# Kernel optimization log

Measured on AMD Instinct MI355X. Metric: run time of the kernel, lower is better.

Reference implementation:

```python
import jax, jax.numpy as jnp
import numpy as np
from jax import lax

K = 3
STRIDE = 1
PAD = 1


def _active_sites(mask):
    # mask: [B, Cm, H, W] int. A patch is 'active' if ANY element of the
    # unfolded (im2col) patch is nonzero -> max-pool of (mask != 0) over the
    # same kernel/stride/padding window.
    m = jnp.any(mask != 0, axis=1, keepdims=True).astype(jnp.float32)  # [B,1,H,W]
    pooled = lax.reduce_window(
        m, 0.0, lax.max,
        window_dimensions=(1, 1, K, K),
        window_strides=(1, 1, STRIDE, STRIDE),
        padding=((0, 0), (0, 0), (PAD, PAD), (PAD, PAD)))
    return pooled > 0  # [B,1,H_out,W_out] bool


def reference(x, mask, weight, bias):
    # Faithful math of MyConv: conv2d(x, weight) + bias at active patch sites
    # (patches whose mask window contains any nonzero), exact zeros elsewhere.
    # masked_scatter in the original preserves patch order, so this equals
    # active * (conv + bias).
    conv = lax.conv_general_dilated(
        x, weight,
        window_strides=(STRIDE, STRIDE),
        padding=((PAD, PAD), (PAD, PAD)),
        dimension_numbers=('NCHW', 'OIHW', 'NCHW'))  # [B,C_out,H_out,W_out]
    active = _active_sites(mask)
    out = (conv + bias[None, :, None, None]) * active.astype(conv.dtype)
    return out


def setup_inputs() -> dict:
    key = jax.random.key(0)
    k1, k2, k3, k4 = jax.random.split(key, 4)
    B, C_in, C_out, H, W = 8, 128, 128, 128, 128
    x = jax.random.normal(k1, (B, C_in, H, W), dtype=jnp.float32)
    mask = jax.random.randint(k2, (B, 1, H, W), 0, 2, dtype=jnp.int32)
    fan_in = C_in * K * K
    bound = 1.0 / np.sqrt(fan_in)
    weight = jax.random.uniform(k3, (C_out, C_in, K, K), minval=-bound, maxval=bound, dtype=jnp.float32)
    bias = jax.random.uniform(k4, (C_out,), minval=-bound, maxval=bound, dtype=jnp.float32)
    return {"x": x, "mask": mask, "weight": weight, "bias": bias}
```

## Files before the change

### kernel.cpp

```cpp
#include <hip/hip_runtime.h>


typedef __bf16 bf16x8 __attribute__((ext_vector_type(8)));
typedef unsigned short u16x8 __attribute__((ext_vector_type(8)));
typedef float f32x4 __attribute__((ext_vector_type(4)));

__device__ __forceinline__ unsigned short f2bf(float f) {
    unsigned int u = __float_as_uint(f);
    u += 0x7fffu + ((u >> 16) & 1u);
    return (unsigned short)(u >> 16);
}

__global__ void cvt_x2(const float* __restrict__ x, unsigned short* __restrict__ xp) {
    const int t   = threadIdx.x;
    const int b   = blockIdx.x / 130;
    const int hh2 = blockIdx.x % 130;
    unsigned short* dst = xp + (size_t)((b * 130 + hh2) * 4) * 4160;
    const u16x8 z = {0, 0, 0, 0, 0, 0, 0, 0};
    if (hh2 == 0 || hh2 == 129) {
        for (int i = t; i < 2080; i += 256) ((u16x8*)dst)[i] = z;
        return;
    }
    const int h  = hh2 - 1;
    const int hf = t >> 7;
    const int w  = t & 127;
    #pragma unroll
    for (int cb = 0; cb < 4; ++cb) {
        unsigned short* slab = dst + cb * 4160;
        if (t < 2) {
            unsigned short* gr = slab + (t == 0 ? 0 : 129) * 32;
            ((u16x8*)gr)[0] = z; ((u16x8*)gr)[1] = z;
            ((u16x8*)gr)[2] = z; ((u16x8*)gr)[3] = z;
        }
        u16x8 v0, v1;
        #pragma unroll
        for (int s = 0; s < 8; ++s)
            v0[s] = f2bf(x[((b * 128 + cb * 32 + hf * 16 + s) * 128 + h) * 128 + w]);
        #pragma unroll
        for (int s = 0; s < 8; ++s)
            v1[s] = f2bf(x[((b * 128 + cb * 32 + hf * 16 + 8 + s) * 128 + h) * 128 + w]);
        *(u16x8*)(slab + (1 + w) * 32 + hf * 16)     = v0;
        *(u16x8*)(slab + (1 + w) * 32 + hf * 16 + 8) = v1;
    }
}

__global__ void pack_w2(const float* __restrict__ wgt, unsigned short* __restrict__ wp) {
    const int e    = blockIdx.x * 256 + threadIdx.x;
    const int j    = e & 31;
    const int m    = (e >> 5) & 127;
    const int r    = e >> 12;
    const int kw   = r - (r / 3) * 3;
    const int cbkh = r / 3;
    const int cb   = cbkh & 3;
    const int kh   = cbkh >> 2;
    const int ci   = cb * 32 + j;
    wp[e] = f2bf(wgt[((m * 128 + ci) * 3 + kh) * 3 + kw]);
}

__global__ __launch_bounds__(256, 4)
void myconv3(const unsigned short* __restrict__ xp,
             const int* __restrict__ mask,
             const unsigned short* __restrict__ wp,
             const float* __restrict__ bias,
             float* __restrict__ out)
{
    __shared__ unsigned short As[3 * 128 * 32];
    __shared__ unsigned short Xs[130 * 32];
    __shared__ float act[128];

    const int t   = threadIdx.x;
    const int blk = blockIdx.x;
    const int b   = blk >> 7;
    const int h   = blk & 127;

    if (t < 128) {
        int any = 0;
        #pragma unroll
        for (int kh = 0; kh < 3; ++kh) {
            int hh = h + kh - 1;
            if ((unsigned)hh < 128u) {
                const int* mrow = mask + (b * 128 + hh) * 128;
                #pragma unroll
                for (int kw = 0; kw < 3; ++kw) {
                    int ww = t + kw - 1;
                    if ((unsigned)ww < 128u) any |= mrow[ww];
                }
            }
        }
        act[t] = any ? 1.0f : 0.0f;
    }

    const int lane = t & 63;
    const int l16  = lane & 15;
    const int q    = lane >> 4;
    const int wv   = t >> 6;
    const int wm   = (wv >> 1) << 6;
    const int wn   = (wv & 1) << 6;

    f32x4 acc[4][4];
    const f32x4 fzero = {0.f, 0.f, 0.f, 0.f};
    #pragma unroll
    for (int i = 0; i < 4; ++i)
        #pragma unroll
        for (int j = 0; j < 4; ++j)
            acc[i][j] = fzero;

    const unsigned char* wpB = (const unsigned char*)wp;
    const unsigned char* xpB = (const unsigned char*)xp;

    for (int kh = 0; kh < 3; ++kh) {
        for (int cb = 0; cb < 4; ++cb) {
            __syncthreads();

            {
                const unsigned char* ga =
                    wpB + (kh * 4 + cb) * 24576 + wv * 6144 + lane * 16;
                #pragma unroll
                for (int u = 0; u < 6; ++u)
                    __builtin_amdgcn_global_load_lds(
                        (const __attribute__((address_space(1))) unsigned int*)(ga + u * 1024),
                        (__attribute__((address_space(3))) unsigned int*)((unsigned char*)As + wv * 6144 + u * 1024),
                        16, 0, 0);
            }
            {
                const unsigned char* gx =
                    xpB + (size_t)(((b * 130 + h + kh) * 4 + cb)) * 8320;
                #pragma unroll
                for (int u = 0; u < 2; ++u)
                    __builtin_amdgcn_global_load_lds(
                        (const __attribute__((address_space(1))) unsigned int*)(gx + wv * 2048 + u * 1024 + lane * 16),
                        (__attribute__((address_space(3))) unsigned int*)((unsigned char*)Xs + wv * 2048 + u * 1024),
                        16, 0, 0);
                if (t < 8)
                    __builtin_amdgcn_global_load_lds(
                        (const __attribute__((address_space(1))) unsigned int*)(gx + 8192 + t * 16),
                        (__attribute__((address_space(3))) unsigned int*)((unsigned char*)Xs + 8192),
                        16, 0, 0);
            }

            __syncthreads();

            #pragma unroll
            for (int kw = 0; kw < 3; ++kw) {
                bf16x8 af[4], bfr[4];
                #pragma unroll
                for (int i = 0; i < 4; ++i)
                    af[i] = *(const bf16x8*)&As[kw * 4096 + (wm + (i << 4) + l16) * 32 + (q << 3)];
                #pragma unroll
                for (int j = 0; j < 4; ++j)
                    bfr[j] = *(const bf16x8*)&Xs[(wn + (j << 4) + l16 + kw) * 32 + (q << 3)];
                #pragma unroll
                for (int i = 0; i < 4; ++i)
                    #pragma unroll
                    for (int j = 0; j < 4; ++j)
                        acc[i][j] = __builtin_amdgcn_mfma_f32_16x16x32_bf16(af[i], bfr[j], acc[i][j], 0, 0, 0);
            }
        }
    }

    #pragma unroll
    for (int i = 0; i < 4; ++i) {
        #pragma unroll
        for (int j = 0; j < 4; ++j) {
            const int ncol = wn + (j << 4) + l16;
            const float a  = act[ncol];
            #pragma unroll
            for (int rg = 0; rg < 4; ++rg) {
                const int m = wm + (i << 4) + (q << 2) + rg;
                out[(((b << 7) + m) << 14) + (h << 7) + ncol] =
                    (acc[i][j][rg] + bias[m]) * a;
            }
        }
    }
}

#define LDAF 40
__global__ __launch_bounds__(256, 2)
void myconv_fb(const float* __restrict__ x,
               const int* __restrict__ mask,
               const float* __restrict__ wgt,
               const float* __restrict__ bias,
               float* __restrict__ out)
{
    __shared__ unsigned short As[128 * LDAF];
    __shared__ unsigned short Bs[128 * LDAF];
    __shared__ float act[128];

    const int t   = threadIdx.x;
    const int blk = blockIdx.x;
    const int b   = blk >> 7;
    const int h   = blk & 127;

    if (t < 128) {
        int any = 0;
        #pragma unroll
        for (int kh = 0; kh < 3; ++kh) {
            int hh = h + kh - 1;
            if ((unsigned)hh < 128u) {
                const int* mrow = mask + (b * 128 + hh) * 128;
                #pragma unroll
                for (int kw = 0; kw < 3; ++kw) {
                    int ww = t + kw - 1;
                    if ((unsigned)ww < 128u) any |= mrow[ww];
                }
            }
        }
        act[t] = any ? 1.0f : 0.0f;
    }

    const int lane = t & 63;
    const int l16  = lane & 15;
    const int half = lane >> 4;
    const int wv   = t >> 6;
    const int wm   = (wv >> 1) << 6;
    const int wn   = (wv & 1) << 6;

    f32x4 acc[4][4];
    const f32x4 fzero = {0.f, 0.f, 0.f, 0.f};
    #pragma unroll
    for (int i = 0; i < 4; ++i)
        #pragma unroll
        for (int j = 0; j < 4; ++j)
            acc[i][j] = fzero;

    const int am  = t >> 3;
    const int ac4 = (t & 7) << 2;
    const int n     = t & 127;
    const int khalf = __builtin_amdgcn_readfirstlane(t >> 7);
    const int xb    = b << 21;

    for (int kt = 0; kt < 36; ++kt) {
        __syncthreads();
        #pragma unroll
        for (int jj = 0; jj < 4; ++jj) {
            const int m = am + (jj << 5);
            const float4 v = *(const float4*)(wgt + m * 1152 + kt * 32 + ac4);
            unsigned short* dst = &As[m * LDAF + ac4];
            dst[0] = f2bf(v.x); dst[1] = f2bf(v.y); dst[2] = f2bf(v.z); dst[3] = f2bf(v.w);
        }
        u16x8 bv0, bv1;
        #pragma unroll
        for (int s = 0; s < 16; ++s) {
            const int k  = kt * 32 + khalf * 16 + s;
            const int ci = (k * 7282) >> 16;
            const int r  = k - ci * 9;
            const int kh = (r >= 3) + (r >= 6);
            const int kw = r - kh * 3;
            const int hh = h + kh - 1;
            float v = 0.f;
            if ((unsigned)hh < 128u) {
                const int ww = n + kw - 1;
                if ((unsigned)ww < 128u)
                    v = x[xb + (ci << 14) + (hh << 7) + ww];
            }
            if (s < 8) bv0[s] = f2bf(v); else bv1[s - 8] = f2bf(v);
        }
        *(u16x8*)&Bs[n * LDAF + khalf * 16]     = bv0;
        *(u16x8*)&Bs[n * LDAF + khalf * 16 + 8] = bv1;

        __syncthreads();

        bf16x8 af[4], bfr[4];
        #pragma unroll
        for (int i = 0; i < 4; ++i)
            af[i] = *(const bf16x8*)&As[(wm + (i << 4) + l16) * LDAF + (half << 3)];
        #pragma unroll
        for (int j = 0; j < 4; ++j)
            bfr[j] = *(const bf16x8*)&Bs[(wn + (j << 4) + l16) * LDAF + (half << 3)];
        #pragma unroll
        for (int i = 0; i < 4; ++i)
            #pragma unroll
            for (int j = 0; j < 4; ++j)
                acc[i][j] = __builtin_amdgcn_mfma_f32_16x16x32_bf16(af[i], bfr[j], acc[i][j], 0, 0, 0);
    }

    #pragma unroll
    for (int i = 0; i < 4; ++i) {
        #pragma unroll
        for (int j = 0; j < 4; ++j) {
            const int ncol = wn + (j << 4) + l16;
            const float a  = act[ncol];
            #pragma unroll
            for (int rg = 0; rg < 4; ++rg) {
                const int m = wm + (i << 4) + (half << 2) + rg;
                out[(((b << 7) + m) << 14) + (h << 7) + ncol] =
                    (acc[i][j][rg] + bias[m]) * a;
            }
        }
    }
}

extern "C" void kernel_launch(void* const* d_in, const int* in_sizes, int n_in,
                              void* d_out, int out_size, void* d_ws, size_t ws_size,
                              hipStream_t stream) {
    const float* x    = (const float*)d_in[0];
    const int*   mask = (const int*)d_in[1];
    const float* wgt  = (const float*)d_in[2];
    const float* bias = (const float*)d_in[3];
    float* out        = (float*)d_out;

    const size_t XP_ELEMS = 8ull * 130 * 4 * 130 * 32;
    const size_t WP_ELEMS = 36ull * 128 * 32;
    const size_t need = (XP_ELEMS + WP_ELEMS) * 2;

    if (ws_size >= need) {
        unsigned short* xpw = (unsigned short*)d_ws;
        unsigned short* wpw = xpw + XP_ELEMS;
        cvt_x2<<<dim3(1040), dim3(256), 0, stream>>>(x, xpw);
        pack_w2<<<dim3(576), dim3(256), 0, stream>>>(wgt, wpw);
        myconv3<<<dim3(1024), dim3(256), 0, stream>>>(xpw, mask, wpw, bias, out);
    } else {
        myconv_fb<<<dim3(1024), dim3(256), 0, stream>>>(x, mask, wgt, bias, out);
    }
}
```

Before: 157.8 us.

## Process two output rows per block, read weights from global, swizzle padded input

The conversion kernel is rewritten to read the input with coalesced float4 loads, transpose through shared memory, and write a cb-major padded layout with an XOR swizzle on the 16-byte chunks. The conv kernel now computes two output rows per block, 512 blocks with 8 N-tiles per wave, so each weight fragment feeds twice as many MFMAs. Weights are loaded straight from global/L2 into registers instead of being staged in LDS. The aim is to cut LDS traffic and bank conflicts and to halve weight reloads per output, at the cost of more accumulator registers, lower occupancy (launch bounds 2) and exposed global-load latency on the weight fragments.

```diff
diff --git a/kernel.cpp b/kernel.cpp
--- a/kernel.cpp
+++ b/kernel.cpp
@@ -11,36 +11,44 @@
     return (unsigned short)(u >> 16);
 }
 
-__global__ void cvt_x2(const float* __restrict__ x, unsigned short* __restrict__ xp) {
+__global__ void cvt_x3(const float* __restrict__ x, unsigned short* __restrict__ xp) {
+    __shared__ float Lf[32 * 132];
     const int t   = threadIdx.x;
-    const int b   = blockIdx.x / 130;
     const int hh2 = blockIdx.x % 130;
-    unsigned short* dst = xp + (size_t)((b * 130 + hh2) * 4) * 4160;
+    const int cb  = (blockIdx.x / 130) & 3;
+    const int b   = blockIdx.x / 520;
+    u16x8* slab = (u16x8*)(xp + (size_t)(((b * 4 + cb) * 130 + hh2)) * 4160);
     const u16x8 z = {0, 0, 0, 0, 0, 0, 0, 0};
+
     if (hh2 == 0 || hh2 == 129) {
-        for (int i = t; i < 2080; i += 256) ((u16x8*)dst)[i] = z;
+        for (int k = t; k < 520; k += 256) slab[k] = z;
         return;
     }
-    const int h  = hh2 - 1;
-    const int hf = t >> 7;
-    const int w  = t & 127;
-    #pragma unroll
-    for (int cb = 0; cb < 4; ++cb) {
-        unsigned short* slab = dst + cb * 4160;
-        if (t < 2) {
-            unsigned short* gr = slab + (t == 0 ? 0 : 129) * 32;
-            ((u16x8*)gr)[0] = z; ((u16x8*)gr)[1] = z;
-            ((u16x8*)gr)[2] = z; ((u16x8*)gr)[3] = z;
-        }
-        u16x8 v0, v1;
-        #pragma unroll
-        for (int s = 0; s < 8; ++s)
-            v0[s] = f2bf(x[((b * 128 + cb * 32 + hf * 16 + s) * 128 + h) * 128 + w]);
-        #pragma unroll
-        for (int s = 0; s < 8; ++s)
-            v1[s] = f2bf(x[((b * 128 + cb * 32 + hf * 16 + 8 + s) * 128 + h) * 128 + w]);
-        *(u16x8*)(slab + (1 + w) * 32 + hf * 16)     = v0;
-        *(u16x8*)(slab + (1 + w) * 32 + hf * 16 + 8) = v1;
+    const int h = hh2 - 1;
+
+    #pragma unroll
+    for (int u = 0; u < 4; ++u) {
+        const int f  = t + 256 * u;
+        const int ci = f >> 5;
+        const int w4 = f & 31;
+        const float4 v = *(const float4*)(x + (((b * 128 + cb * 32 + ci) * 128 + h) << 7) + (w4 << 2));
+        *(float4*)&Lf[ci * 132 + (w4 << 2)] = v;
+    }
+    __syncthreads();
+
+    for (int k = t; k < 520; k += 256) {
+        const int r = k >> 2;
+        const int c = k & 3;
+        u16x8 o;
+        if (r == 0 || r == 129) {
+            o = z;
+        } else {
+            const int w   = r - 1;
+            const int ci0 = (c ^ (r & 3)) << 3;
+            #pragma unroll
+            for (int s = 0; s < 8; ++s) o[s] = f2bf(Lf[(ci0 + s) * 132 + w]);
+        }
+        slab[k] = o;
     }
 }
 
@@ -57,23 +65,24 @@
     wp[e] = f2bf(wgt[((m * 128 + ci) * 3 + kh) * 3 + kw]);
 }
 
-__global__ __launch_bounds__(256, 4)
-void myconv3(const unsigned short* __restrict__ xp,
+__global__ __launch_bounds__(256, 2)
+void myconv4(const unsigned short* __restrict__ xp,
              const int* __restrict__ mask,
              const unsigned short* __restrict__ wp,
              const float* __restrict__ bias,
              float* __restrict__ out)
 {
-    __shared__ unsigned short As[3 * 128 * 32];
-    __shared__ unsigned short Xs[130 * 32];
-    __shared__ float act[128];
-
-    const int t   = threadIdx.x;
-    const int blk = blockIdx.x;
-    const int b   = blk >> 7;
-    const int h   = blk & 127;
-
-    if (t < 128) {
+    __shared__ unsigned char Xs[16640];
+    __shared__ float act[256];
+
+    const int t  = threadIdx.x;
+    const int b  = blockIdx.x >> 6;
+    const int h0 = (blockIdx.x & 63) << 1;
+
+    {
+        const int g = t >> 7;
+        const int w = t & 127;
+        const int h = h0 + g;
         int any = 0;
         #pragma unroll
         for (int kh = 0; kh < 3; ++kh) {
@@ -82,7 +91,7 @@
                 const int* mrow = mask + (b * 128 + hh) * 128;
                 #pragma unroll
                 for (int kw = 0; kw < 3; ++kw) {
-                    int ww = t + kw - 1;
+                    int ww = w + kw - 1;
                     if ((unsigned)ww < 128u) any |= mrow[ww];
                 }
             }
@@ -94,65 +103,60 @@
     const int l16  = lane & 15;
     const int q    = lane >> 4;
     const int wv   = t >> 6;
-    const int wm   = (wv >> 1) << 6;
-    const int wn   = (wv & 1) << 6;
-
-    f32x4 acc[4][4];
+    const int wm   = (wv & 1) << 6;
+    const int g    = wv >> 1;
+
+    f32x4 acc[4][8];
     const f32x4 fzero = {0.f, 0.f, 0.f, 0.f};
     #pragma unroll
     for (int i = 0; i < 4; ++i)
         #pragma unroll
-        for (int j = 0; j < 4; ++j)
+        for (int j = 0; j < 8; ++j)
             acc[i][j] = fzero;
 
-    const unsigned char* wpB = (const unsigned char*)wp;
+    int bb[3];
+    #pragma unroll
+    for (int kw = 0; kw < 3; ++kw)
+        bb[kw] = g * 8320 + (l16 + kw) * 64 + ((q ^ ((l16 + kw) & 3)) << 4);
+
+    const unsigned char* agl = (const unsigned char*)wp + (wm + l16) * 64 + q * 16;
     const unsigned char* xpB = (const unsigned char*)xp;
 
     for (int kh = 0; kh < 3; ++kh) {
         for (int cb = 0; cb < 4; ++cb) {
             __syncthreads();
 
-            {
-                const unsigned char* ga =
-                    wpB + (kh * 4 + cb) * 24576 + wv * 6144 + lane * 16;
-                #pragma unroll
-                for (int u = 0; u < 6; ++u)
-                    __builtin_amdgcn_global_load_lds(
-                        (const __attribute__((address_space(1))) unsigned int*)(ga + u * 1024),
-                        (__attribute__((address_space(3))) unsigned int*)((unsigned char*)As + wv * 6144 + u * 1024),
-                        16, 0, 0);
-            }
-            {
-                const unsigned char* gx =
-                    xpB + (size_t)(((b * 130 + h + kh) * 4 + cb)) * 8320;
-                #pragma unroll
-                for (int u = 0; u < 2; ++u)
-                    __builtin_amdgcn_global_load_lds(
-                        (const __attribute__((address_space(1))) unsigned int*)(gx + wv * 2048 + u * 1024 + lane * 16),
-                        (__attribute__((address_space(3))) unsigned int*)((unsigned char*)Xs + wv * 2048 + u * 1024),
-                        16, 0, 0);
-                if (t < 8)
-                    __builtin_amdgcn_global_load_lds(
-                        (const __attribute__((address_space(1))) unsigned int*)(gx + 8192 + t * 16),
-                        (__attribute__((address_space(3))) unsigned int*)((unsigned char*)Xs + 8192),
-                        16, 0, 0);
-            }
+            const unsigned char* gx =
+                xpB + (size_t)((b * 4 + cb) * 130 + h0 + kh) * 8320;
+            #pragma unroll
+            for (int u = 0; u < 4; ++u)
+                __builtin_amdgcn_global_load_lds(
+                    (const __attribute__((address_space(1))) unsigned int*)(gx + ((wv << 2) + u) * 1024 + lane * 16),
+                    (__attribute__((address_space(3))) unsigned int*)(Xs + ((wv << 2) + u) * 1024),
+                    16, 0, 0);
+            if (t < 16)
+                __builtin_amdgcn_global_load_lds(
+                    (const __attribute__((address_space(1))) unsigned int*)(gx + 16384 + t * 16),
+                    (__attribute__((address_space(3))) unsigned int*)(Xs + 16384),
+                    16, 0, 0);
 
             __syncthreads();
 
+            const unsigned char* ar = agl + (kh * 4 + cb) * 24576;
             #pragma unroll
             for (int kw = 0; kw < 3; ++kw) {
-                bf16x8 af[4], bfr[4];
+                bf16x8 af[4];
                 #pragma unroll
                 for (int i = 0; i < 4; ++i)
-                    af[i] = *(const bf16x8*)&As[kw * 4096 + (wm + (i << 4) + l16) * 32 + (q << 3)];
-                #pragma unroll
-                for (int j = 0; j < 4; ++j)
-                    bfr[j] = *(const bf16x8*)&Xs[(wn + (j << 4) + l16 + kw) * 32 + (q << 3)];
+                    af[i] = *(const bf16x8*)(ar + kw * 8192 + i * 1024);
+                bf16x8 bfr[8];
+                #pragma unroll
+                for (int j = 0; j < 8; ++j)
+                    bfr[j] = *(const bf16x8*)(Xs + bb[kw] + j * 1024);
                 #pragma unroll
                 for (int i = 0; i < 4; ++i)
                     #pragma unroll
-                    for (int j = 0; j < 4; ++j)
+                    for (int j = 0; j < 8; ++j)
                         acc[i][j] = __builtin_amdgcn_mfma_f32_16x16x32_bf16(af[i], bfr[j], acc[i][j], 0, 0, 0);
             }
         }
@@ -160,16 +164,15 @@
 
     #pragma unroll
     for (int i = 0; i < 4; ++i) {
-        #pragma unroll
-        for (int j = 0; j < 4; ++j) {
-            const int ncol = wn + (j << 4) + l16;
-            const float a  = act[ncol];
-            #pragma unroll
-            for (int rg = 0; rg < 4; ++rg) {
-                const int m = wm + (i << 4) + (q << 2) + rg;
-                out[(((b << 7) + m) << 14) + (h << 7) + ncol] =
-                    (acc[i][j][rg] + bias[m]) * a;
-            }
+        const f32x4 bv = *(const f32x4*)(bias + wm + (i << 4) + (q << 2));
+        #pragma unroll
+        for (int j = 0; j < 8; ++j) {
+            const int w = (j << 4) + l16;
+            const float a = act[(g << 7) + w];
+            float* base = out + (((((b << 7) + wm + (i << 4) + (q << 2)) << 7) + h0 + g) << 7) + w;
+            #pragma unroll
+            for (int rg = 0; rg < 4; ++rg)
+                base[rg << 14] = (acc[i][j][rg] + bv[rg]) * a;
         }
     }
 }
@@ -299,16 +302,16 @@
     const float* bias = (const float*)d_in[3];
     float* out        = (float*)d_out;
 
-    const size_t XP_ELEMS = 8ull * 130 * 4 * 130 * 32;
+    const size_t XP_ELEMS = 4160ull * 4160;
     const size_t WP_ELEMS = 36ull * 128 * 32;
     const size_t need = (XP_ELEMS + WP_ELEMS) * 2;
 
     if (ws_size >= need) {
         unsigned short* xpw = (unsigned short*)d_ws;
         unsigned short* wpw = xpw + XP_ELEMS;
-        cvt_x2<<<dim3(1040), dim3(256), 0, stream>>>(x, xpw);
+        cvt_x3<<<dim3(4160), dim3(256), 0, stream>>>(x, xpw);
         pack_w2<<<dim3(576), dim3(256), 0, stream>>>(wgt, wpw);
-        myconv3<<<dim3(1024), dim3(256), 0, stream>>>(xpw, mask, wpw, bias, out);
+        myconv4<<<dim3(512), dim3(256), 0, stream>>>(xpw, mask, wpw, bias, out);
     } else {
         myconv_fb<<<dim3(1024), dim3(256), 0, stream>>>(x, mask, wgt, bias, out);
     }
```

Result: no change. 155.3 us (-1.6%).
